# Kernel optimization log

Measured on AMD Instinct MI355X. Metric: run time of the kernel, lower is better.

Reference implementation:

```python
import jax, jax.numpy as jnp
import numpy as np
import math

B, T, C = 2, 2048, 1024
H = 16
D = C // H  # 64


def setup_inputs() -> dict:
    key = jax.random.key(0)
    k1, k2, k3 = jax.random.split(key, 3)
    x = jax.random.normal(k1, (B, T, C), dtype=jnp.float32)
    W_attn = jax.random.normal(k2, (3 * C, C), dtype=jnp.float32) * (1.0 / math.sqrt(C))
    W_proj = jax.random.normal(k3, (C, C), dtype=jnp.float32) * (1.0 / math.sqrt(C))
    return {"x": x, "W_attn": W_attn, "W_proj": W_proj}


def reference(x, W_attn, W_proj):
    b, t, c = x.shape
    qkv = x @ W_attn.T                       # [B,T,3C]
    q, k, v = jnp.split(qkv, 3, axis=2)
    # [B,H,T,D]
    q = q.reshape(b, t, H, D).transpose(0, 2, 1, 3)
    k = k.reshape(b, t, H, D).transpose(0, 2, 1, 3)
    v = v.reshape(b, t, H, D).transpose(0, 2, 1, 3)
    scale = 1.0 / math.sqrt(D)
    P = jnp.einsum('bhqd,bhkd->bhqk', q, k) * scale   # [B,H,T,T]
    S = jax.nn.sigmoid(P)
    causal = jnp.tril(jnp.ones((t, t), dtype=bool))   # [T,T]
    S_lower = jnp.where(causal, S, 0.0)
    # suffix (reverse) cumulative sum along key axis
    Z = jax.lax.cumsum(S_lower, axis=3, reverse=True)
    P_prime = P - Z
    P_masked = jnp.where(causal, P_prime, -jnp.inf)
    att = jax.nn.softmax(P_masked, axis=-1)
    y = jnp.einsum('bhqk,bhkd->bhqd', att, v)         # [B,H,T,D]
    y = y.transpose(0, 2, 1, 3).reshape(b, t, c)
    return y @ W_proj.T
```

## Files before the change

kernel.cpp:

```cpp
#include <hip/hip_runtime.h>


typedef _Float16 h8 __attribute__((ext_vector_type(8)));
typedef _Float16 h4 __attribute__((ext_vector_type(4)));
typedef float f4 __attribute__((ext_vector_type(4)));

template <int CTRL>
__device__ __forceinline__ float dpp_shr_self(float x) {
  int xi = __builtin_bit_cast(int, x);
  return __builtin_bit_cast(float,
      __builtin_amdgcn_update_dpp(xi, xi, CTRL, 0xF, 0xF, false));
}
__device__ __forceinline__ float scan16_max(float x) {
  x = fmaxf(x, dpp_shr_self<0x111>(x));
  x = fmaxf(x, dpp_shr_self<0x112>(x));
  x = fmaxf(x, dpp_shr_self<0x114>(x));
  x = fmaxf(x, dpp_shr_self<0x118>(x));
  return x;
}
__device__ __forceinline__ float bcast15(float x) {
  return __builtin_bit_cast(float,
      __builtin_amdgcn_ds_swizzle(__builtin_bit_cast(int, x), 0x01F0));
}

__device__ __forceinline__ void gload_lds16(const _Float16* src, _Float16* dst_lds) {
  __builtin_amdgcn_global_load_lds(
      (const __attribute__((address_space(1))) void*)src,
      (__attribute__((address_space(3))) void*)dst_lds, 16, 0, 0);
}

__global__ __launch_bounds__(256) void convert_all_kernel(const float* __restrict__ x,
                                                          const float* __restrict__ Wa,
                                                          const float* __restrict__ Wp,
                                                          _Float16* __restrict__ xh,
                                                          _Float16* __restrict__ wah,
                                                          _Float16* __restrict__ wph) {
  int i = blockIdx.x * 256 + threadIdx.x;
  const float* src;
  _Float16* dst;
  int off;
  if (i < 1048576) { src = x; dst = xh; off = i; }
  else if (i < 1048576 + 786432) { src = Wa; dst = wah; off = i - 1048576; }
  else { src = Wp; dst = wph; off = i - (1048576 + 786432); }
  f4 v = *(const f4*)(src + (size_t)off * 4);
  h4 o;
  for (int j = 0; j < 4; ++j) o[j] = (_Float16)v[j];
  *(h4*)(dst + (size_t)off * 4) = o;
}

template <int BM, int BN, int STRIPE, typename OutT>
__global__ __launch_bounds__(256) void gemm_nt_kernel(const _Float16* __restrict__ A,
                                                      const _Float16* __restrict__ B,
                                                      OutT* __restrict__ C,
                                                      int M, int N, int K) {
  constexpr int MI = BM / 32;
  constexpr int NI = BN / 32;
  __shared__ _Float16 As[BM * 64];
  __shared__ _Float16 Bs[BN * 64];
  const int tid = threadIdx.x;
  const int wave = tid >> 6, lane = tid & 63;
  const int wm = wave >> 1, wn = wave & 1;
  const int l16 = lane & 15, q4 = lane >> 4;
  const int lrow = lane >> 3, lsc = lane & 7;

  const int xcd = blockIdx.x & 7;
  const int idx = blockIdx.x >> 3;
  const int n_blk = xcd * STRIPE + idx % STRIPE;
  const int m_blk = idx / STRIPE;
  const int m0 = m_blk * BM, n0 = n_blk * BN;

  f4 acc[MI][NI] = {};

  for (int k0 = 0; k0 < K; k0 += 64) {
    __syncthreads();
#pragma unroll
    for (int j = 0; j < MI; ++j) {
      const int row = j * 32 + wave * 8 + lrow;
      gload_lds16(A + (size_t)(m0 + row) * K + k0 + (lsc ^ (row & 7)) * 8,
                  As + j * 2048 + wave * 512);
    }
#pragma unroll
    for (int j = 0; j < NI; ++j) {
      const int row = j * 32 + wave * 8 + lrow;
      gload_lds16(B + (size_t)(n0 + row) * K + k0 + (lsc ^ (row & 7)) * 8,
                  Bs + j * 2048 + wave * 512);
    }
    __syncthreads();
#pragma unroll
    for (int ks = 0; ks < 2; ++ks) {
      h8 af[MI], bf[NI];
#pragma unroll
      for (int mi = 0; mi < MI; ++mi) {
        const int row = wm * (BM / 2) + mi * 16 + l16;
        af[mi] = *(const h8*)(As + row * 64 + ((ks * 4 + q4) ^ (row & 7)) * 8);
      }
#pragma unroll
      for (int ni = 0; ni < NI; ++ni) {
        const int row = wn * (BN / 2) + ni * 16 + l16;
        bf[ni] = *(const h8*)(Bs + row * 64 + ((ks * 4 + q4) ^ (row & 7)) * 8);
      }
#pragma unroll
      for (int mi = 0; mi < MI; ++mi)
#pragma unroll
        for (int ni = 0; ni < NI; ++ni)
          acc[mi][ni] = __builtin_amdgcn_mfma_f32_16x16x32_f16(af[mi], bf[ni], acc[mi][ni], 0, 0, 0);
    }
  }
#pragma unroll
  for (int mi = 0; mi < MI; ++mi)
#pragma unroll
    for (int ni = 0; ni < NI; ++ni)
#pragma unroll
      for (int i = 0; i < 4; ++i) {
        int m = m0 + wm * (BM / 2) + mi * 16 + q4 * 4 + i;
        int n = n0 + wn * (BN / 2) + ni * 16 + l16;
        C[(size_t)m * N + n] = (OutT)acc[mi][ni][i];
      }
}

__global__ __launch_bounds__(256, 4) void attn_kernel(const _Float16* __restrict__ qkv,
                                                      _Float16* __restrict__ yh) {
  __shared__ _Float16 Qs[64 * 72];
  __shared__ _Float16 Ks[64 * 72];
  __shared__ _Float16 Vt[64 * 72];
  __shared__ _Float16 Ss[64 * 72];

  const int tid = threadIdx.x;
  const int wave = tid >> 6, lane = tid & 63;
  const int l16 = lane & 15, q = lane >> 4;
  const int qt = 31 - (blockIdx.x >> 5);
  const int bh = blockIdx.x & 31;
  const int b = bh >> 4, h = bh & 15;
  const size_t base = (size_t)b * 2048 * 3072 + h * 64;
  const int rl = 16 * wave + 4 * q;
  const int kt0 = (qt >= 1) ? (qt - 1) : 0;

  h8 Ua, Ub, ONES;
#pragma unroll
  for (int j = 0; j < 8; ++j) {
    int kp = q * 8 + j;
    Ua[j]   = (kp < l16)      ? (_Float16)1.f : (_Float16)0.f;
    Ub[j]   = (kp < 16 + l16) ? (_Float16)1.f : (_Float16)0.f;
    ONES[j] = (_Float16)1.f;
  }

  const int srow0 = tid >> 3, sc8 = tid & 7;
  const int srow1 = srow0 + 32;
  {
    const _Float16 qscale = (_Float16)0.18033688f;
    h8 q0 = *(const h8*)(qkv + base + (size_t)(qt * 64 + srow0) * 3072 + sc8 * 8);
    h8 q1 = *(const h8*)(qkv + base + (size_t)(qt * 64 + srow1) * 3072 + sc8 * 8);
    for (int e = 0; e < 8; ++e) { q0[e] = q0[e] * qscale; q1[e] = q1[e] * qscale; }
    *(h8*)(Qs + srow0 * 72 + sc8 * 8) = q0;
    *(h8*)(Qs + srow1 * 72 + sc8 * 8) = q1;
  }

  h8 kr0, kr1, vr0, vr1;
  {
    const _Float16* kg = qkv + base + (size_t)kt0 * 64 * 3072 + 1024;
    kr0 = *(const h8*)(kg + (size_t)srow0 * 3072 + sc8 * 8);
    kr1 = *(const h8*)(kg + (size_t)srow1 * 3072 + sc8 * 8);
    const _Float16* vg = qkv + base + (size_t)kt0 * 64 * 3072 + 2048 + lane;
    for (int j = 0; j < 8; ++j) vr0[j] = vg[(size_t)(wave * 16 + j) * 3072];
    for (int j = 0; j < 8; ++j) vr1[j] = vg[(size_t)(wave * 16 + 8 + j) * 3072];
  }

  f4 Oacc[4] = {};
  float m_r[4], l_r[4], c_r[4];
#pragma unroll
  for (int i = 0; i < 4; ++i) { m_r[i] = -1e30f; l_r[i] = 0.f; c_r[i] = 0.f; }

  for (int kt = kt0; kt <= qt; ++kt) {
    __syncthreads();
    *(h8*)(Ks + srow0 * 72 + sc8 * 8) = kr0;
    *(h8*)(Ks + srow1 * 72 + sc8 * 8) = kr1;
    *(h8*)(Vt + lane * 72 + wave * 16) = vr0;
    *(h8*)(Vt + lane * 72 + wave * 16 + 8) = vr1;
    __syncthreads();

    if (kt < qt) {
      const _Float16* kg = qkv + base + (size_t)(kt + 1) * 64 * 3072 + 1024;
      kr0 = *(const h8*)(kg + (size_t)srow0 * 3072 + sc8 * 8);
      kr1 = *(const h8*)(kg + (size_t)srow1 * 3072 + sc8 * 8);
      const _Float16* vg = qkv + base + (size_t)(kt + 1) * 64 * 3072 + 2048 + lane;
      for (int j = 0; j < 8; ++j) vr0[j] = vg[(size_t)(wave * 16 + j) * 3072];
      for (int j = 0; j < 8; ++j) vr1[j] = vg[(size_t)(wave * 16 + 8 + j) * 3072];
    }
    const bool diag = (kt == qt);

    f4 pacc[4] = {};
#pragma unroll
    for (int ks = 0; ks < 2; ++ks) {
      h8 af = *(const h8*)(Qs + (16 * wave + l16) * 72 + ks * 32 + q * 8);
#pragma unroll
      for (int ni = 0; ni < 4; ++ni) {
        h8 bf = *(const h8*)(Ks + (16 * ni + l16) * 72 + ks * 32 + q * 8);
        pacc[ni] = __builtin_amdgcn_mfma_f32_16x16x32_f16(af, bf, pacc[ni], 0, 0, 0);
      }
    }

#pragma unroll
    for (int ni = 0; ni < 4; ++ni) {
      const int col = 16 * ni + l16;
#pragma unroll
      for (int i = 0; i < 4; ++i) {
        float e = __builtin_amdgcn_exp2f(-pacc[ni][i]);
        float s = __builtin_amdgcn_rcpf(1.f + e) * 1.44269504f;
        if (diag && col > rl + i) s = 0.f;
        Ss[(rl + i) * 72 + col] = (_Float16)s;
      }
    }
    f4 ex[4], tot;
    {
      h8 s0 = *(const h8*)(Ss + (16 * wave + l16) * 72 + q * 8);
      h8 s1 = *(const h8*)(Ss + (16 * wave + l16) * 72 + 32 + q * 8);
      f4 z = {};
      f4 t0 = __builtin_amdgcn_mfma_f32_16x16x32_f16(s0, ONES, z, 0, 0, 0);
      ex[0] = __builtin_amdgcn_mfma_f32_16x16x32_f16(s0, Ua, z, 0, 0, 0);
      ex[1] = __builtin_amdgcn_mfma_f32_16x16x32_f16(s0, Ub, z, 0, 0, 0);
      ex[2] = __builtin_amdgcn_mfma_f32_16x16x32_f16(s1, Ua, t0, 0, 0, 0);
      ex[3] = __builtin_amdgcn_mfma_f32_16x16x32_f16(s1, Ub, t0, 0, 0, 0);
      tot   = __builtin_amdgcn_mfma_f32_16x16x32_f16(s1, ONES, t0, 0, 0, 0);
    }
    float rmax[4];
#pragma unroll
    for (int i = 0; i < 4; ++i) {
      float L0 = pacc[0][i] + (c_r[i] + ex[0][i]);
      float L1 = pacc[1][i] + (c_r[i] + ex[1][i]);
      float L2 = pacc[2][i] + (c_r[i] + ex[2][i]);
      float L3 = pacc[3][i] + (c_r[i] + ex[3][i]);
      if (diag) {
        if (0  + l16 > rl + i) L0 = -1e30f;
        if (16 + l16 > rl + i) L1 = -1e30f;
        if (32 + l16 > rl + i) L2 = -1e30f;
        if (48 + l16 > rl + i) L3 = -1e30f;
      }
      pacc[0][i] = L0; pacc[1][i] = L1; pacc[2][i] = L2; pacc[3][i] = L3;
      rmax[i] = fmaxf(fmaxf(L0, L1), fmaxf(L2, L3));
      c_r[i] += tot[i];
    }
    float mn[4], al[4];
#pragma unroll
    for (int i = 0; i < 4; ++i) {
      float gm = bcast15(scan16_max(rmax[i]));
      mn[i] = fmaxf(m_r[i], gm);
      al[i] = __builtin_amdgcn_exp2f(m_r[i] - mn[i]);
      m_r[i] = mn[i];
    }
#pragma unroll
    for (int ni = 0; ni < 4; ++ni)
#pragma unroll
      for (int i = 0; i < 4; ++i) {
        float w = __builtin_amdgcn_exp2f(pacc[ni][i] - mn[i]);
        Ss[(rl + i) * 72 + 16 * ni + l16] = (_Float16)w;
      }
#pragma unroll
    for (int ni = 0; ni < 4; ++ni)
#pragma unroll
      for (int i = 0; i < 4; ++i) Oacc[ni][i] *= al[i];
    {
      h8 w0 = *(const h8*)(Ss + (16 * wave + l16) * 72 + q * 8);
      h8 w1 = *(const h8*)(Ss + (16 * wave + l16) * 72 + 32 + q * 8);
      f4 z = {};
      f4 la = __builtin_amdgcn_mfma_f32_16x16x32_f16(w0, ONES, z, 0, 0, 0);
      la = __builtin_amdgcn_mfma_f32_16x16x32_f16(w1, ONES, la, 0, 0, 0);
#pragma unroll
      for (int i = 0; i < 4; ++i) l_r[i] = l_r[i] * al[i] + la[i];
#pragma unroll
      for (int ni = 0; ni < 4; ++ni) {
        h8 bf0 = *(const h8*)(Vt + (16 * ni + l16) * 72 + q * 8);
        Oacc[ni] = __builtin_amdgcn_mfma_f32_16x16x32_f16(w0, bf0, Oacc[ni], 0, 0, 0);
        h8 bf1 = *(const h8*)(Vt + (16 * ni + l16) * 72 + 32 + q * 8);
        Oacc[ni] = __builtin_amdgcn_mfma_f32_16x16x32_f16(w1, bf1, Oacc[ni], 0, 0, 0);
      }
    }
  }

#pragma unroll
  for (int ni = 0; ni < 4; ++ni)
#pragma unroll
    for (int i = 0; i < 4; ++i) {
      int t = qt * 64 + rl + i;
      float yv = Oacc[ni][i] * __builtin_amdgcn_rcpf(l_r[i]);
      yh[((size_t)(b * 2048 + t)) * 1024 + h * 64 + 16 * ni + l16] = (_Float16)yv;
    }
}

extern "C" void kernel_launch(void* const* d_in, const int* in_sizes, int n_in,
                              void* d_out, int out_size, void* d_ws, size_t ws_size,
                              hipStream_t stream) {
  const float* x  = (const float*)d_in[0];
  const float* Wa = (const float*)d_in[1];
  const float* Wp = (const float*)d_in[2];
  float* out = (float*)d_out;

  char* ws = (char*)d_ws;
  _Float16* xh   = (_Float16*)(ws);
  _Float16* wah  = (_Float16*)(ws + 8388608);
  _Float16* wph  = (_Float16*)(ws + 14680064);
  _Float16* qkvh = (_Float16*)(ws + 16777216);
  _Float16* yh   = (_Float16*)(ws + 41943040);

  convert_all_kernel<<<8192, 256, 0, stream>>>(x, Wa, Wp, xh, wah, wph);

  gemm_nt_kernel<128, 128, 3, _Float16>
      <<<768, 256, 0, stream>>>(xh, wah, qkvh, 4096, 3072, 1024);
  attn_kernel<<<1024, 256, 0, stream>>>(qkvh, yh);
  gemm_nt_kernel<64, 128, 1, float>
      <<<512, 256, 0, stream>>>(yh, wph, out, 4096, 1024, 1024);
}
```

Before: 148.1 us.

## Replace QKV GEMM with double-buffered 256x192 tile kernel using 512 threads

Adds a dedicated QKV projection GEMM that uses 256x192 output tiles, 8 waves per block and double-buffered LDS. Loads for the next K tile are issued directly into LDS while MFMAs run on the current tile, with wave priority raised around the MFMA bursts. The aim is to hide global-load latency and raise per-block data reuse compared with the previous 128x128 single-buffer GEMM. In exchange it needs more LDS (about 112 KB per block), launches only 256 blocks, and writes its output with scattered scalar stores.

```diff
diff --git a/kernel.cpp b/kernel.cpp
--- a/kernel.cpp
+++ b/kernel.cpp
@@ -27,6 +27,11 @@
   __builtin_amdgcn_global_load_lds(
       (const __attribute__((address_space(1))) void*)src,
       (__attribute__((address_space(3))) void*)dst_lds, 16, 0, 0);
+}
+
+__device__ __forceinline__ void vmcnt0_fence() {
+  asm volatile("s_waitcnt vmcnt(0)" ::: "memory");
+  __builtin_amdgcn_sched_barrier(0);
 }
 
 __global__ __launch_bounds__(256) void convert_all_kernel(const float* __restrict__ x,
@@ -48,6 +53,109 @@
   *(h4*)(dst + (size_t)off * 4) = o;
 }
 
+__global__ __launch_bounds__(512, 2) void gemm1_pipe_kernel(const _Float16* __restrict__ A,
+                                                            const _Float16* __restrict__ B,
+                                                            _Float16* __restrict__ C,
+                                                            int M, int N, int K) {
+  __shared__ _Float16 As[2][256 * 64];
+  __shared__ _Float16 Bs[2][192 * 64];
+  const int tid = threadIdx.x;
+  const int wave = tid >> 6, lane = tid & 63;
+  const int wm = wave >> 2, wn = wave & 3;
+  const int l16 = lane & 15, q4 = lane >> 4;
+  const int lrow = lane >> 3, lsc = lane & 7;
+
+  const int xcd = blockIdx.x & 7;
+  const int idx = blockIdx.x >> 3;
+  const int n_blk = xcd * 2 + (idx & 1);
+  const int m_blk = idx >> 1;
+  const int m0 = m_blk * 256, n0 = n_blk * 192;
+
+  f4 acc[8][3] = {};
+
+  const int NT = K >> 6;
+  {
+    const int k0 = 0;
+#pragma unroll
+    for (int j = 0; j < 4; ++j) {
+      const int row = j * 64 + wave * 8 + lrow;
+      gload_lds16(A + (size_t)(m0 + row) * K + k0 + (lsc ^ (row & 7)) * 8,
+                  &As[0][(j * 64 + wave * 8) * 64]);
+    }
+#pragma unroll
+    for (int j = 0; j < 3; ++j) {
+      const int row = j * 64 + wave * 8 + lrow;
+      gload_lds16(B + (size_t)(n0 + row) * K + k0 + (lsc ^ (row & 7)) * 8,
+                  &Bs[0][(j * 64 + wave * 8) * 64]);
+    }
+  }
+  vmcnt0_fence();
+  __builtin_amdgcn_s_barrier();
+
+  int cur = 0;
+  for (int kt = 0; kt < NT; ++kt) {
+    h8 bf[3][2];
+#pragma unroll
+    for (int ni = 0; ni < 3; ++ni)
+#pragma unroll
+      for (int ks = 0; ks < 2; ++ks) {
+        const int row = wn * 48 + ni * 16 + l16;
+        bf[ni][ks] = *(const h8*)(&Bs[cur][row * 64 + ((ks * 4 + q4) ^ (row & 7)) * 8]);
+      }
+    if (kt + 1 < NT) {
+      const int k0 = (kt + 1) * 64;
+      const int nxt = cur ^ 1;
+#pragma unroll
+      for (int j = 0; j < 4; ++j) {
+        const int row = j * 64 + wave * 8 + lrow;
+        gload_lds16(A + (size_t)(m0 + row) * K + k0 + (lsc ^ (row & 7)) * 8,
+                    &As[nxt][(j * 64 + wave * 8) * 64]);
+      }
+#pragma unroll
+      for (int j = 0; j < 3; ++j) {
+        const int row = j * 64 + wave * 8 + lrow;
+        gload_lds16(B + (size_t)(n0 + row) * K + k0 + (lsc ^ (row & 7)) * 8,
+                    &Bs[nxt][(j * 64 + wave * 8) * 64]);
+      }
+    }
+#pragma unroll
+    for (int P = 0; P < 4; ++P) {
+      h8 af[2][2];
+#pragma unroll
+      for (int i = 0; i < 2; ++i)
+#pragma unroll
+        for (int ks = 0; ks < 2; ++ks) {
+          const int row = wm * 128 + (P * 2 + i) * 16 + l16;
+          af[i][ks] = *(const h8*)(&As[cur][row * 64 + ((ks * 4 + q4) ^ (row & 7)) * 8]);
+        }
+      __builtin_amdgcn_s_barrier();
+      __builtin_amdgcn_s_setprio(1);
+#pragma unroll
+      for (int ks = 0; ks < 2; ++ks)
+#pragma unroll
+        for (int i = 0; i < 2; ++i)
+#pragma unroll
+          for (int ni = 0; ni < 3; ++ni)
+            acc[P * 2 + i][ni] = __builtin_amdgcn_mfma_f32_16x16x32_f16(
+                af[i][ks], bf[ni][ks], acc[P * 2 + i][ni], 0, 0, 0);
+      __builtin_amdgcn_s_setprio(0);
+      if (P == 3 && kt + 1 < NT) vmcnt0_fence();
+      __builtin_amdgcn_s_barrier();
+    }
+    cur ^= 1;
+  }
+#pragma unroll
+  for (int mi = 0; mi < 8; ++mi)
+#pragma unroll
+    for (int ni = 0; ni < 3; ++ni)
+#pragma unroll
+      for (int i = 0; i < 4; ++i) {
+        int m = m0 + wm * 128 + mi * 16 + q4 * 4 + i;
+        int n = n0 + wn * 48 + ni * 16 + l16;
+        C[(size_t)m * N + n] = (_Float16)acc[mi][ni][i];
+      }
+}
+
 template <int BM, int BN, int STRIPE, typename OutT>
 __global__ __launch_bounds__(256) void gemm_nt_kernel(const _Float16* __restrict__ A,
                                                       const _Float16* __restrict__ B,
@@ -303,9 +411,10 @@
 
   convert_all_kernel<<<8192, 256, 0, stream>>>(x, Wa, Wp, xh, wah, wph);
 
-  gemm_nt_kernel<128, 128, 3, _Float16>
-      <<<768, 256, 0, stream>>>(xh, wah, qkvh, 4096, 3072, 1024);
+  gemm1_pipe_kernel<<<256, 512, 0, stream>>>(xh, wah, qkvh, 4096, 3072, 1024);
+
   attn_kernel<<<1024, 256, 0, stream>>>(qkvh, yh);
+
   gemm_nt_kernel<64, 128, 1, float>
       <<<512, 256, 0, stream>>>(yh, wph, out, 4096, 1024, 1024);
 }
```

New measurement: 148.5 us. About the same (+0.3%).
